# Performance work log

Measured on AMD Instinct MI355X. Metric: run time of the kernel, lower is better.

## Reference

```python
import jax, jax.numpy as jnp
import numpy as np

B, NPB, K = 8, 4096, 16            # batches, points per batch, knn neighbors
IN_FEAT, OUT_FEAT, N_HEADS = 64, 64, 8
N = B * NPB
HD = OUT_FEAT // N_HEADS           # per-head dim (linear_w output width)
EPS = 1e-5


def _bn(x, g, b):
    # LayerNorm1d == BatchNorm1d over channel dim with stats across (N, k)
    m = jnp.mean(x, axis=(0, 1), keepdims=True)
    v = jnp.mean((x - m) ** 2, axis=(0, 1), keepdims=True)
    return (x - m) * jax.lax.rsqrt(v + EPS) * g + b


def _knn_idx(feat):
    # per-batch self-KNN in feature space (torch_geometric.nn.knn(x, x, k, batch, batch))
    f = feat.reshape(B, NPB, -1)
    sq = jnp.sum(f * f, axis=-1)                               # [B, n]
    d = sq[:, :, None] + sq[:, None, :] - 2.0 * jnp.einsum('bnc,bmc->bnm', f, f)
    _, idx = jax.lax.top_k(-d, K)                              # [B, n, K]
    idx = idx + (jnp.arange(B) * NPB)[:, None, None]           # global indices
    return idx.reshape(N, K)


def setup_inputs() -> dict:
    key = jax.random.key(0)
    ks = jax.random.split(key, 12)
    s = 0.05
    return {
        "p": jax.random.normal(ks[0], (N, 3), dtype=jnp.float32),
        "x": jax.random.normal(ks[1], (N, IN_FEAT), dtype=jnp.float32),
        "o": jnp.full((B,), NPB, dtype=jnp.int32),
        # q/k/v projections
        "wq": jax.random.normal(ks[2], (IN_FEAT, OUT_FEAT)) * s, "bq": jnp.zeros((OUT_FEAT,)),
        "wk": jax.random.normal(ks[3], (IN_FEAT, OUT_FEAT)) * s, "bk": jnp.zeros((OUT_FEAT,)),
        "wv": jax.random.normal(ks[4], (IN_FEAT, OUT_FEAT)) * s, "bv": jnp.zeros((OUT_FEAT,)),
        # linear_p: Linear(3,3) -> BN(3) -> ReLU -> Linear(3, out)
        "wp1": jax.random.normal(ks[5], (3, 3)) * s, "bp1": jnp.zeros((3,)),
        "gp": jnp.ones((3,)), "btp": jnp.zeros((3,)),
        "wp2": jax.random.normal(ks[6], (3, OUT_FEAT)) * s, "bp2": jnp.zeros((OUT_FEAT,)),
        # linear_w: BN(mid) -> ReLU -> Linear(mid, hd) -> BN(hd) -> ReLU -> Linear(hd, hd)
        "g1": jnp.ones((OUT_FEAT,)), "bt1": jnp.zeros((OUT_FEAT,)),
        "ww1": jax.random.normal(ks[7], (OUT_FEAT, HD)) * s, "bw1": jnp.zeros((HD,)),
        "g2": jnp.ones((HD,)), "bt2": jnp.zeros((HD,)),
        "ww2": jax.random.normal(ks[8], (HD, HD)) * s, "bw2": jnp.zeros((HD,)),
    }


def reference(p, x, o, wq, bq, wk, bk, wv, bv, wp1, bp1, gp, btp, wp2, bp2,
              g1, bt1, ww1, bw1, g2, bt2, ww2, bw2):
    # o encodes equal-size batches (NPB each); structure is baked into the knn helper.
    xq = x @ wq + bq                      # [N, mid]
    xk = x @ wk + bk                      # [N, mid]
    xv = x @ wv + bv                      # [N, out]
    idx_k = _knn_idx(xk)                  # KNN in k-feature space
    idx_v = _knn_idx(xv)                  # separate KNN in v-feature space (as in source)
    xk_g = xk[idx_k]                      # [N, K, mid]
    p_rel = p[idx_k] - p[:, None, :]      # grouped relative xyz [N, K, 3]
    xv_g = xv[idx_v]                      # [N, K, out]
    # position encoding MLP
    h = p_rel @ wp1 + bp1
    h = jax.nn.relu(_bn(h, gp, btp))
    p_r = h @ wp2 + bp2                   # [N, K, out]; einops.reduce with i=1 is identity
    # relation features and attention-weight MLP
    r = xk_g - xq[:, None, :] + p_r       # [N, K, mid]
    w = jax.nn.relu(_bn(r, g1, bt1)) @ ww1 + bw1
    w = jax.nn.relu(_bn(w, g2, bt2)) @ ww2 + bw2   # [N, K, HD]
    w = jax.nn.softmax(w, axis=1)         # softmax over neighbors
    comb = (xv_g + p_r).reshape(N, K, N_HEADS, HD)
    out = jnp.einsum('ntsi,nti->nsi', comb, w).reshape(N, OUT_FEAT)
    return out
```

## Files before the change

kernel.cpp:

```cpp
#include <hip/hip_runtime.h>
#include <hip/hip_bf16.h>

typedef __hip_bfloat16 bf16;

#define NPTS  32768
#define NPB   4096
#define NPAIR (NPTS*16)
#define IMASK 32767
#define EPSB  1e-5f

#define O_WQ  0
#define O_BQ  4096
#define O_WK  4160
#define O_BK  8256
#define O_WV  8320
#define O_BV  12416
#define O_WP1 12480
#define O_BP1 12489
#define O_GP  12492
#define O_BTP 12495
#define O_WP2 12498
#define O_BP2 12690
#define O_G1  12754
#define O_BT1 12818
#define O_WW1 12882
#define O_BW1 13394
#define O_G2  13402
#define O_BT2 13410
#define O_WW2 13418
#define O_BW2 13482
#define NPRM  13490

__device__ __forceinline__ float b2f(bf16 v){ return __bfloat162float(v); }
__device__ __forceinline__ float u16f(unsigned short u){ return __uint_as_float(((unsigned)u)<<16); }
__device__ __forceinline__ float ldany(const void* p, long long i, int f32){
    return f32 ? ((const float*)p)[i] : b2f(((const bf16*)p)[i]);
}

__device__ __forceinline__ void split2(float x, unsigned &h, unsigned &m){
    unsigned u  = __float_as_uint(x);
    unsigned hr = (u + 0x7FFFu + ((u>>16)&1u)) & 0xFFFF0000u;
    float xm = x - __uint_as_float(hr);
    h = hr >> 16;
    m = __float_as_uint(xm) >> 16;
}

__device__ __forceinline__ void gll16(const void* g, void* l){
    __builtin_amdgcn_global_load_lds((const __attribute__((address_space(1))) unsigned*)(g),
                                     (__attribute__((address_space(3))) unsigned*)(l), 16, 0, 0);
}
__device__ __forceinline__ void gll4(const void* g, void* l){
    __builtin_amdgcn_global_load_lds((const __attribute__((address_space(1))) unsigned*)(g),
                                     (__attribute__((address_space(3))) unsigned*)(l), 4, 0, 0);
}

struct P20 { const void* p[20]; };

__global__ __launch_bounds__(256) void k_conv(P20 t, const void* __restrict__ p,
                                              const void* __restrict__ x, const void* __restrict__ wq0,
                                              float* __restrict__ prm, float* __restrict__ p32,
                                              int* __restrict__ flags)
{
    __shared__ float red[2][4];
    const unsigned short* xu = (const unsigned short*)x;
    const unsigned short* wu = (const unsigned short*)wq0;
    const int tid = threadIdx.x, lane = tid & 63, wvi = tid >> 6;
    float mx = fabsf(u16f(xu[tid]));
    float mw = fabsf(u16f(wu[tid]));
    for (int off = 32; off; off >>= 1){
        mx = fmaxf(mx, __shfl_down(mx, off));
        mw = fmaxf(mw, __shfl_down(mw, off));
    }
    if (lane == 0){ red[0][wvi] = mx; red[1][wvi] = mw; }
    __syncthreads();
    const float ax = fmaxf(fmaxf(red[0][0], red[0][1]), fmaxf(red[0][2], red[0][3]));
    const float aw = fmaxf(fmaxf(red[1][0], red[1][1]), fmaxf(red[1][2], red[1][3]));
    const int f0 = (ax > 1e6f) ? 1 : 0;
    const int f1 = (aw > 1e6f) ? 1 : 0;
    if (blockIdx.x == 0 && tid == 0){ flags[0] = f0; flags[1] = f1; }
    const int i = blockIdx.x*256 + tid;
    if (i < NPRM){
        const int sz[20] = {4096,64,4096,64,4096,64,9,3,3,3,192,64,64,64,512,8,8,8,64,8};
        int seg = 0, rem = i;
        while (rem >= sz[seg]){ rem -= sz[seg]; ++seg; }
        prm[i] = ldany(t.p[seg], rem, f1);
    } else {
        const int j = i - NPRM;
        if (j < NPTS*3) p32[j] = ldany(p, j, f0);
    }
}

__global__ __launch_bounds__(192) void k_proj(
    const void* __restrict__ x, const int* __restrict__ flags,
    const float* __restrict__ prm,
    float* __restrict__ xq, float* __restrict__ xk, float* __restrict__ xv,
    float* __restrict__ sqk, float* __restrict__ sqv,
    unsigned* __restrict__ hkp, unsigned* __restrict__ mkp,
    unsigned* __restrict__ hvp, unsigned* __restrict__ mvp)
{
    const int tid = threadIdx.x, lane = tid & 63, wvi = tid >> 6;
    const int f32 = flags[0];
    const int OW = (wvi==0) ? O_WQ : (wvi==1) ? O_WK : O_WV;
    const int OB = (wvi==0) ? O_BQ : (wvi==1) ? O_BK : O_BV;
    float Wc[64];
    #pragma unroll
    for (int k = 0; k < 64; ++k) Wc[k] = prm[OW + k*64 + lane];
    const float bias = prm[OB + lane];
    float* outp = (wvi==0) ? xq : (wvi==1) ? xk : xv;
    const int ptbase = blockIdx.x*32;
    for (int it = 0; it < 32; ++it){
        const int pt = ptbase + it;
        float xl = ldany(x, (long long)pt*64 + lane, f32);
        float acc = bias;
        #pragma unroll
        for (int k = 0; k < 64; ++k) acc += __shfl(xl, k)*Wc[k];
        outp[(size_t)pt*64 + lane] = acc;
        if (wvi){
            unsigned h16, m16; split2(acc, h16, m16);
            unsigned hn = __shfl_down(h16,1), mn = __shfl_down(m16,1);
            if (!(lane & 1)){
                const int u = lane >> 3, pos = u ^ (pt & 7);
                const size_t gi = (size_t)pt*32 + pos*4 + ((lane & 7) >> 1);
                if (wvi == 1){ hkp[gi] = h16 | (hn<<16);  mkp[gi] = m16 | (mn<<16); }
                else         { hvp[gi] = h16 | (hn<<16);  mvp[gi] = m16 | (mn<<16); }
            }
            float s = acc*acc;
            for (int off=32; off; off>>=1) s += __shfl_down(s, off);
            if (lane == 0){ if (wvi == 1) sqk[pt] = s; else sqv[pt] = s; }
        }
    }
}


using bfrag  = __attribute__((ext_vector_type(8))) short;
using f32x16 = __attribute__((ext_vector_type(16))) float;

__device__ __forceinline__ int lds_sw(int row, int unit){
    return (row<<6) + (((unit ^ row) & 7)<<3);
}

__global__ __launch_bounds__(256, 4) void k_knn_part(
    const float* __restrict__ featk, const float* __restrict__ featv,
    const unsigned* __restrict__ hkp, const unsigned* __restrict__ mkp,
    const unsigned* __restrict__ hvp, const unsigned* __restrict__ mvp,
    const float* __restrict__ sqk, const float* __restrict__ sqv,
    const float* __restrict__ p32, const float* __restrict__ prm,
    int* __restrict__ idx_k, int* __restrict__ idx_v,
    float* __restrict__ part1)
{
    __shared__ __attribute__((aligned(16))) unsigned char smem[34048];
    __shared__ float bn1red[4][6];
    unsigned short* Ch = (unsigned short*)smem;
    unsigned short* Cm = (unsigned short*)(smem + 8192);
    float* Dt  = (float*)(smem + 16384);
    float* sqC = (float*)(smem + 16384 + 17408);
    unsigned long long* Lbuf = (unsigned long long*)smem;

    const int tid = threadIdx.x;
    const int swz = ((int)blockIdx.x & 7) * 128 + ((int)blockIdx.x >> 3);
    const int kid = swz >> 9;
    const int bid = swz & 511;
    const float*    feat = kid ? featv : featk;
    const float*    sq   = kid ? sqv  : sqk;
    const unsigned* hpl  = kid ? hvp : hkp;
    const unsigned* mpl  = kid ? mvp : mkp;
    const int b  = bid >> 6;
    const int qt = bid & 63;
    const int q0 = b*NPB + qt*64;
    const int cb = b*NPB;

    const int lane = tid & 63, wv = tid >> 6;
    const int qg = wv >> 1, cg = wv & 1;
    const int l31 = lane & 31, hi = lane >> 5;
    const int selq = (wv << 4) + (lane >> 2);
    const int sub  = lane & 3;
    const int owner = lane & ~3;

    bfrag qh[4], qm[4];
    {
        const int qr = q0 + (qg<<5) + l31;
        #pragma unroll
        for (int ks = 0; ks < 4; ++ks){
            const int u = ks*2 + hi;
            const int pos = u ^ (qr & 7);
            union { uint4 u4; bfrag v; } ch, cm;
            ch.u4 = *(const uint4*)&hpl[(size_t)qr*32 + pos*4];
            cm.u4 = *(const uint4*)&mpl[(size_t)qr*32 + pos*4];
            qh[ks] = ch.v; qm[ks] = cm.v;
        }
    }

    float d5[5]; int i5[5];
    #pragma unroll
    for (int i=0;i<5;++i){ d5[i] = 3.4e38f; i5[i] = 0; }

    const unsigned* hrowA = hpl + (size_t)cb*32 + (size_t)tid*4;
    const unsigned* mrowA = mpl + (size_t)cb*32 + (size_t)tid*4;

    #define STAGE(CHN) { \
        const size_t co = (size_t)(CHN)*2048; \
        gll16(hrowA + co,        (void*)&Ch[8*tid]); \
        gll16(hrowA + co + 1024, (void*)&Ch[8*tid + 2048]); \
        gll16(mrowA + co,        (void*)&Cm[8*tid]); \
        gll16(mrowA + co + 1024, (void*)&Cm[8*tid + 2048]); \
        if (tid < 64) gll4(sq + cb + (CHN)*64 + tid, (void*)&sqC[tid]); \
    }

    #define MFMA_PHASE() { \
        const int cd = (cg<<5) + l31; \
        f32x16 acc = {0.f,0.f,0.f,0.f,0.f,0.f,0.f,0.f,0.f,0.f,0.f,0.f,0.f,0.f,0.f,0.f}; \
        _Pragma("unroll") \
        for (int ks = 0; ks < 4; ++ks){ \
            const int u = ks*2 + hi; \
            union { uint4 u4; bfrag v; } bh, bm; \
            bh.u4 = *(const uint4*)&Ch[lds_sw(cd, u)]; \
            bm.u4 = *(const uint4*)&Cm[lds_sw(cd, u)]; \
            acc = __builtin_amdgcn_mfma_f32_32x32x16_bf16(qm[ks], bm.v, acc, 0, 0, 0); \
            acc = __builtin_amdgcn_mfma_f32_32x32x16_bf16(qh[ks], bm.v, acc, 0, 0, 0); \
            acc = __builtin_amdgcn_mfma_f32_32x32x16_bf16(qm[ks], bh.v, acc, 0, 0, 0); \
            acc = __builtin_amdgcn_mfma_f32_32x32x16_bf16(qh[ks], bh.v, acc, 0, 0, 0); \
        } \
        const float sc = sqC[(cg<<5) + l31]; \
        _Pragma("unroll") \
        for (int i = 0; i < 16; ++i){ \
            const int row = (qg<<5) + (i&3) + 8*(i>>2) + 4*hi; \
            Dt[row*68 + (cg<<5) + l31] = sc - 2.f*acc[i]; \
        } }

    STAGE(0)
    __syncthreads();

    for (int chn = 0; chn < 64; ++chn){
        MFMA_PHASE()
        __syncthreads();
        if (chn + 1 < 64) STAGE(chn+1)
        {
            float worst = __shfl(d5[4], owner+3);
            unsigned m16 = 0;
            const int rowoff = selq*68 + sub*16;
            #pragma unroll
            for (int r = 0; r < 4; ++r){
                float4 v = *(const float4*)&Dt[rowoff + 4*r];
                m16 |= (v.x < worst ? 1u : 0u) << (4*r+0);
                m16 |= (v.y < worst ? 1u : 0u) << (4*r+1);
                m16 |= (v.z < worst ? 1u : 0u) << (4*r+2);
                m16 |= (v.w < worst ? 1u : 0u) << (4*r+3);
            }
            unsigned ma = __shfl(m16, owner+0), mb = __shfl(m16, owner+1);
            unsigned mc = __shfl(m16, owner+2), md = __shfl(m16, owner+3);
            unsigned long long m = (unsigned long long)ma
                                 | ((unsigned long long)mb << 16)
                                 | ((unsigned long long)mc << 32)
                                 | ((unsigned long long)md << 48);
            const int qrow = selq*68;
            const int c0 = cb + chn*64;
            const int prevlane = (lane - 1) & 63;
            while (m){
                int c = (int)__builtin_ctzll(m); m &= m - 1;
                float d = Dt[qrow + c];
                int gi = c0 + c;
                float pl = __shfl(d5[4], prevlane);
                int   pi = __shfl(i5[4], prevlane);
                bool takePrev = (sub != 0) && (pl > d);
                float v  = takePrev ? pl : d;
                int   vi = takePrev ? pi : gi;
                #pragma unroll
                for (int i = 4; i >= 1; --i){
                    bool sh   = d5[i-1] > v;
                    bool here = !sh && (d5[i] > v);
                    d5[i] = sh ? d5[i-1] : (here ? v  : d5[i]);
                    i5[i] = sh ? i5[i-1] : (here ? vi : i5[i]);
                }
                bool h0 = d5[0] > v;
                d5[0] = h0 ? v  : d5[0];
                i5[0] = h0 ? vi : i5[0];
            }
        }
        __syncthreads();
    }
    #undef MFMA_PHASE
    #undef STAGE

    unsigned long long k5[5];
    {
        const float* qrow = feat + (size_t)(q0 + selq)*64;
        #pragma unroll
        for (int s = 0; s < 5; ++s){
            const int gi = i5[s];
            const float* crow = feat + (size_t)gi*64;
            float acc = 0.f;
            #pragma unroll
            for (int k4 = 0; k4 < 16; ++k4){
                float4 qv = *(const float4*)&qrow[4*k4];
                float4 cv = *(const float4*)&crow[4*k4];
                acc += qv.x*cv.x; acc += qv.y*cv.y; acc += qv.z*cv.z; acc += qv.w*cv.w;
            }
            float d = sq[gi] - 2.f*acc;
            unsigned ud = __float_as_uint(d);
            ud ^= (ud & 0x80000000u) ? 0xFFFFFFFFu : 0x80000000u;
            k5[s] = ((unsigned long long)ud << 32) | (unsigned)gi;
        }
    }
    #pragma unroll
    for (int pass = 0; pass < 5; ++pass){
        #pragma unroll
        for (int i = (pass & 1); i + 1 < 5; i += 2){
            unsigned long long a = k5[i], bb = k5[i+1];
            bool sw = a > bb;
            k5[i]   = sw ? bb : a;
            k5[i+1] = sw ? a : bb;
        }
    }
    __syncthreads();
    #pragma unroll
    for (int j = 0; j < 5; ++j) Lbuf[(size_t)tid*6 + j] = k5[j];
    Lbuf[(size_t)tid*6 + 5] = ~0ull;
    __syncthreads();
    int fi[16];
    #pragma unroll
    for (int i = 0; i < 16; ++i) fi[i] = 0;
    if (sub == 0){
        const unsigned long long* L0 = &Lbuf[(size_t)(tid+0)*6];
        const unsigned long long* L1 = &Lbuf[(size_t)(tid+1)*6];
        const unsigned long long* L2 = &Lbuf[(size_t)(tid+2)*6];
        const unsigned long long* L3 = &Lbuf[(size_t)(tid+3)*6];
        int p0 = 0, p1 = 0, p2 = 0, p3 = 0;
        #pragma unroll
        for (int o = 0; o < 16; ++o){
            unsigned long long b0 = L0[p0], b1v = L1[p1], b2v = L2[p2], b3v = L3[p3];
            unsigned long long m01 = (b0  < b1v) ? b0  : b1v;  int s01 = (b0  < b1v) ? 0 : 1;
            unsigned long long m23 = (b2v < b3v) ? b2v : b3v;  int s23 = (b2v < b3v) ? 2 : 3;
            unsigned long long mm  = (m01 < m23) ? m01 : m23;  int ss  = (m01 < m23) ? s01 : s23;
            fi[o] = (int)(unsigned)(mm & 0xFFFFFFFFull);
            if      (ss == 0) ++p0;
            else if (ss == 1) ++p1;
            else if (ss == 2) ++p2;
            else              ++p3;
        }
        int* idx_out = kid ? idx_v : idx_k;
        #pragma unroll
        for (int i4 = 0; i4 < 4; ++i4)
            *(int4*)&idx_out[(size_t)(q0+selq)*16 + 4*i4] =
                make_int4(fi[4*i4], fi[4*i4+1], fi[4*i4+2], fi[4*i4+3]);
    }

    if (kid == 0){
        const float w00=prm[O_WP1+0], w01=prm[O_WP1+1], w02=prm[O_WP1+2];
        const float w10=prm[O_WP1+3], w11=prm[O_WP1+4], w12=prm[O_WP1+5];
        const float w20=prm[O_WP1+6], w21=prm[O_WP1+7], w22=prm[O_WP1+8];
        const float bb0=prm[O_BP1+0], bb1=prm[O_BP1+1], bb2=prm[O_BP1+2];
        const size_t gq = (size_t)(q0 + selq);
        const float px=p32[gq*3+0], py=p32[gq*3+1], pz=p32[gq*3+2];
        float s0=0.f,s1=0.f,s2=0.f,t0=0.f,t1=0.f,t2=0.f;
        #pragma unroll
        for (int o = 0; o < 16; ++o){
            int gi = __shfl(fi[o], owner);
            if ((o & 3) == sub){
                const int j = gi & IMASK;
                float rx = p32[j*3+0]-px, ry = p32[j*3+1]-py, rz = p32[j*3+2]-pz;
                float h0 = bb0 + rx*w00 + ry*w10 + rz*w20;
                float h1 = bb1 + rx*w01 + ry*w11 + rz*w21;
                float h2 = bb2 + rx*w02 + ry*w12 + rz*w22;
                s0+=h0; s1+=h1; s2+=h2; t0+=h0*h0; t1+=h1*h1; t2+=h2*h2;
            }
        }
        #pragma unroll
        for (int off = 1; off < 64; off <<= 1){
            s0+=__shfl_down(s0,off); s1+=__shfl_down(s1,off); s2+=__shfl_down(s2,off);
            t0+=__shfl_down(t0,off); t1+=__shfl_down(t1,off); t2+=__shfl_down(t2,off);
        }
        if (lane == 0){
            bn1red[wv][0]=s0; bn1red[wv][1]=s1; bn1red[wv][2]=s2;
            bn1red[wv][3]=t0; bn1red[wv][4]=t1; bn1red[wv][5]=t2;
        }
        __syncthreads();
        if (tid < 6)
            part1[(size_t)tid*512 + bid] =
                bn1red[0][tid]+bn1red[1][tid]+bn1red[2][tid]+bn1red[3][tid];
    }
}

__global__ __launch_bounds__(256) void k_bnred_par(
    const float* __restrict__ part, int G, int C,
    const float* __restrict__ gamma, const float* __restrict__ beta,
    float* __restrict__ aff, float invCount)
{
    __shared__ float rs[4], rq[4];
    const int c = blockIdx.x;
    const int tid = threadIdx.x;
    float s = 0.f, q = 0.f;
    for (int g = tid; g < G; g += 256){
        s += part[(size_t)c*G + g];
        q += part[(size_t)(C+c)*G + g];
    }
    for (int off=32; off; off>>=1){ s += __shfl_down(s,off); q += __shfl_down(q,off); }
    if ((tid & 63) == 0){ rs[tid>>6] = s; rq[tid>>6] = q; }
    __syncthreads();
    if (tid == 0){
        float S = rs[0]+rs[1]+rs[2]+rs[3], Q = rq[0]+rq[1]+rq[2]+rq[3];
        float mean = S*invCount;
        float var  = fmaxf(Q*invCount - mean*mean, 0.f);
        float sc = gamma[c] * rsqrtf(var + EPSB);
        aff[c]   = sc;
        aff[C+c] = beta[c] - mean*sc;
    }
}

__global__ __launch_bounds__(256) void k_rstats(
    const float* __restrict__ p32,
    const float* __restrict__ xq, const float* __restrict__ xk, const int* __restrict__ idx_k,
    const float* __restrict__ bn1aff, const float* __restrict__ prm,
    float* __restrict__ part2)
{
    const int tid = threadIdx.x, lane = tid & 63, wvi = tid >> 6;
    const float wa = prm[O_WP2+lane], wb = prm[O_WP2+64+lane], wc = prm[O_WP2+128+lane];
    const float bpc = prm[O_BP2+lane];
    const float w00=prm[O_WP1+0], w01=prm[O_WP1+1], w02=prm[O_WP1+2];
    const float w10=prm[O_WP1+3], w11=prm[O_WP1+4], w12=prm[O_WP1+5];
    const float w20=prm[O_WP1+6], w21=prm[O_WP1+7], w22=prm[O_WP1+8];
    const float bb0=prm[O_BP1+0], bb1=prm[O_BP1+1], bb2=prm[O_BP1+2];
    const float sc0=bn1aff[0], sc1=bn1aff[1], sc2=bn1aff[2];
    const float sh0=bn1aff[3], sh1=bn1aff[4], sh2=bn1aff[5];
    const int base = (blockIdx.x*4 + wvi) * 64;
    float asum=0.f, asq=0.f;
    float px=0.f, py=0.f, pz=0.f, xql=0.f;
    for (int e4 = 0; e4 < 16; ++e4){
        const int gb = base + e4*4;
        if ((gb & 15) == 0){
            const int n = gb >> 4;
            px=p32[n*3+0]; py=p32[n*3+1]; pz=p32[n*3+2];
            xql = xq[(size_t)n*64+lane];
        }
        int4 jj = *(const int4*)&idx_k[gb];
        int j[4] = { jj.x & IMASK, jj.y & IMASK, jj.z & IMASK, jj.w & IMASK };
        float kx[4], qx[4][3];
        #pragma unroll
        for (int u=0;u<4;++u){
            qx[u][0]=p32[j[u]*3+0]; qx[u][1]=p32[j[u]*3+1]; qx[u][2]=p32[j[u]*3+2];
            kx[u] = xk[(size_t)j[u]*64+lane];
        }
        #pragma unroll
        for (int u=0;u<4;++u){
            float rx = qx[u][0]-px, ry = qx[u][1]-py, rz = qx[u][2]-pz;
            float h0 = bb0 + rx*w00 + ry*w10 + rz*w20;
            float h1 = bb1 + rx*w01 + ry*w11 + rz*w21;
            float h2 = bb2 + rx*w02 + ry*w12 + rz*w22;
            float r0 = fmaxf(h0*sc0+sh0, 0.f), r1 = fmaxf(h1*sc1+sh1,0.f), r2 = fmaxf(h2*sc2+sh2,0.f);
            float pr = r0*wa + r1*wb + r2*wc + bpc;
            float rv = kx[u] - xql + pr;
            asum += rv; asq += rv*rv;
        }
    }
    __shared__ float red[4][128];
    red[wvi][lane] = asum; red[wvi][64+lane] = asq;
    __syncthreads();
    if (tid < 128)
        part2[(size_t)tid*2048 + blockIdx.x] = red[0][tid]+red[1][tid]+red[2][tid]+red[3][tid];
}

__global__ __launch_bounds__(256) void k_wstats(
    const float* __restrict__ p32,
    const float* __restrict__ xq, const float* __restrict__ xk, const int* __restrict__ idx_k,
    const float* __restrict__ bn1aff, const float* __restrict__ prm,
    const float* __restrict__ bn2aff, float* __restrict__ wbuf, float* __restrict__ part3)
{
    __shared__ float4 PRW[64];
    __shared__ float2 SS2[64];
    __shared__ float4 W1A[64], W1B[64];
    const int tid = threadIdx.x;
    if (tid < 64){
        PRW[tid] = make_float4(prm[O_WP2+tid], prm[O_WP2+64+tid], prm[O_WP2+128+tid], prm[O_BP2+tid]);
        SS2[tid] = make_float2(bn2aff[tid], bn2aff[64+tid]);
        W1A[tid] = make_float4(prm[O_WW1+tid*8+0],prm[O_WW1+tid*8+1],prm[O_WW1+tid*8+2],prm[O_WW1+tid*8+3]);
        W1B[tid] = make_float4(prm[O_WW1+tid*8+4],prm[O_WW1+tid*8+5],prm[O_WW1+tid*8+6],prm[O_WW1+tid*8+7]);
    }
    __syncthreads();
    const int g = blockIdx.x*256 + tid;
    const int n = g >> 4;
    const int j = idx_k[g] & IMASK;
    const float w00=prm[O_WP1+0], w01=prm[O_WP1+1], w02=prm[O_WP1+2];
    const float w10=prm[O_WP1+3], w11=prm[O_WP1+4], w12=prm[O_WP1+5];
    const float w20=prm[O_WP1+6], w21=prm[O_WP1+7], w22=prm[O_WP1+8];
    const float bb0=prm[O_BP1+0], bb1=prm[O_BP1+1], bb2=prm[O_BP1+2];
    const float sc0=bn1aff[0], sc1=bn1aff[1], sc2=bn1aff[2];
    const float sh0=bn1aff[3], sh1=bn1aff[4], sh2=bn1aff[5];
    float rx = p32[j*3+0] - p32[n*3+0];
    float ry = p32[j*3+1] - p32[n*3+1];
    float rz = p32[j*3+2] - p32[n*3+2];
    float h0 = bb0 + rx*w00 + ry*w10 + rz*w20;
    float h1 = bb1 + rx*w01 + ry*w11 + rz*w21;
    float h2 = bb2 + rx*w02 + ry*w12 + rz*w22;
    float r0 = fmaxf(h0*sc0+sh0, 0.f), r1 = fmaxf(h1*sc1+sh1,0.f), r2 = fmaxf(h2*sc2+sh2,0.f);
    float wacc[8];
    #pragma unroll
    for (int i=0;i<8;++i) wacc[i] = prm[O_BW1+i];
    const float4* kr = (const float4*)(xk + (size_t)j*64);
    const float4* qr = (const float4*)(xq + (size_t)n*64);
    #pragma unroll
    for (int c4=0;c4<16;++c4){
        float4 kv = kr[c4], qv = qr[c4];
        float kvv[4] = {kv.x,kv.y,kv.z,kv.w};
        float qvv[4] = {qv.x,qv.y,qv.z,qv.w};
        #pragma unroll
        for (int d=0; d<4; ++d){
            int c = 4*c4 + d;
            float4 pw = PRW[c]; float2 ss = SS2[c];
            float pr = r0*pw.x + r1*pw.y + r2*pw.z + pw.w;
            float rr = kvv[d] - qvv[d] + pr;
            float y = fmaxf(rr*ss.x + ss.y, 0.f);
            float4 wA = W1A[c], wB = W1B[c];
            wacc[0]+=y*wA.x; wacc[1]+=y*wA.y; wacc[2]+=y*wA.z; wacc[3]+=y*wA.w;
            wacc[4]+=y*wB.x; wacc[5]+=y*wB.y; wacc[6]+=y*wB.z; wacc[7]+=y*wB.w;
        }
    }
    *(float4*)&wbuf[(size_t)g*8]   = make_float4(wacc[0],wacc[1],wacc[2],wacc[3]);
    *(float4*)&wbuf[(size_t)g*8+4] = make_float4(wacc[4],wacc[5],wacc[6],wacc[7]);
    float st[16];
    #pragma unroll
    for (int i=0;i<8;++i){ st[i]=wacc[i]; st[8+i]=wacc[i]*wacc[i]; }
    for (int off=32; off; off>>=1){
        #pragma unroll
        for (int k=0;k<16;++k) st[k] += __shfl_down(st[k], off);
    }
    __shared__ float red[4][16];
    const int lane = tid&63, wvi = tid>>6;
    if (lane==0){
        #pragma unroll
        for (int k=0;k<16;++k) red[wvi][k]=st[k];
    }
    __syncthreads();
    if (tid < 16)
        part3[(size_t)tid*2048 + blockIdx.x] = red[0][tid]+red[1][tid]+red[2][tid]+red[3][tid];
}

__global__ __launch_bounds__(256) void k_out(
    const float* __restrict__ p32, const float* __restrict__ xv,
    const int* __restrict__ idx_k, const int* __restrict__ idx_v,
    const float* __restrict__ bn1aff, const float* __restrict__ prm,
    const float* __restrict__ wbuf, const float* __restrict__ bn3aff,
    const int* __restrict__ flags, void* __restrict__ out)
{
    const int tid = threadIdx.x, lane = tid & 63, wvi = tid >> 6;
    const int n = blockIdx.x*4 + wvi;
    const int f32 = flags[0];
    const float w00=prm[O_WP1+0], w01=prm[O_WP1+1], w02=prm[O_WP1+2];
    const float w10=prm[O_WP1+3], w11=prm[O_WP1+4], w12=prm[O_WP1+5];
    const float w20=prm[O_WP1+6], w21=prm[O_WP1+7], w22=prm[O_WP1+8];
    const float bb0=prm[O_BP1+0], bb1=prm[O_BP1+1], bb2=prm[O_BP1+2];
    const float sc0=bn1aff[0], sc1=bn1aff[1], sc2=bn1aff[2];
    const float sh0=bn1aff[3], sh1=bn1aff[4], sh2=bn1aff[5];
    const float wa=prm[O_WP2+lane], wb=prm[O_WP2+64+lane], wc=prm[O_WP2+128+lane];
    const float bpc=prm[O_BP2+lane];
    const int i = lane & 7;
    float s3[8], t3[8], w2col[8];
    #pragma unroll
    for (int m=0;m<8;++m){
        s3[m]=bn3aff[m]; t3[m]=bn3aff[8+m];
        w2col[m]=prm[O_WW2+m*8+i];
    }
    const float bw2i = prm[O_BW2+i];
    const float px=p32[n*3+0], py=p32[n*3+1], pz=p32[n*3+2];
    float comb[16], wf[16];
    #pragma unroll
    for (int t=0;t<16;++t){
        const int g = n*16 + t;
        const int jk = idx_k[g] & IMASK;
        const int jv = idx_v[g] & IMASK;
        float rx=p32[jk*3+0]-px, ry=p32[jk*3+1]-py, rz=p32[jk*3+2]-pz;
        float h0=bb0+rx*w00+ry*w10+rz*w20;
        float h1=bb1+rx*w01+ry*w11+rz*w21;
        float h2=bb2+rx*w02+ry*w12+rz*w22;
        float r0=fmaxf(h0*sc0+sh0,0.f), r1=fmaxf(h1*sc1+sh1,0.f), r2=fmaxf(h2*sc2+sh2,0.f);
        float pr=r0*wa+r1*wb+r2*wc+bpc;
        float4 wA = *(const float4*)&wbuf[(size_t)g*8];
        float4 wB = *(const float4*)&wbuf[(size_t)g*8+4];
        float wm[8] = {wA.x,wA.y,wA.z,wA.w,wB.x,wB.y,wB.z,wB.w};
        float acc = bw2i;
        #pragma unroll
        for (int m=0;m<8;++m){
            float y3 = fmaxf(wm[m]*s3[m]+t3[m],0.f);
            acc += y3*w2col[m];
        }
        wf[t]=acc;
        comb[t]=xv[(size_t)jv*64+lane]+pr;
    }
    float mx = wf[0];
    #pragma unroll
    for (int t=1;t<16;++t) mx = fmaxf(mx, wf[t]);
    float ssum=0.f, osum=0.f;
    #pragma unroll
    for (int t=0;t<16;++t){ float e = __expf(wf[t]-mx); ssum += e; osum += e*comb[t]; }
    const float v = osum / ssum;
    if (f32) ((float*)out)[(size_t)n*64+lane] = v;
    else     ((bf16*)out)[(size_t)n*64+lane] = __float2bfloat16(v);
}

extern "C" void kernel_launch(void* const* d_in, const int* in_sizes, int n_in,
                              void* d_out, int out_size, void* d_ws, size_t ws_size,
                              hipStream_t stream)
{
    const void* p  = d_in[0];
    const void* x  = d_in[1];
    P20 prms;
    for (int i = 0; i < 20; ++i) prms.p[i] = d_in[3+i];

    float* W = (float*)d_ws;
    float* xqf    = W + 0;
    float* xkf    = W + 2097152;
    float* xvf    = W + 4194304;
    float* sqk    = W + 6291456;
    float* sqv    = W + 6324224;
    int*   idx_k  = (int*)(W + 6356992);
    int*   idx_v  = (int*)(W + 6881280);
    float* p32    = W + 7405568;
    float* prm    = W + 7503872;
    float* part1  = W + 7517376;
    float* part2  = W + 7529664;
    float* part3  = W + 7791808;
    float* bn1aff = W + 7824576;
    float* bn2aff = W + 7824592;
    float* bn3aff = W + 7824720;
    int*   flags  = (int*)(W + 7824736);
    unsigned* hkp = (unsigned*)(W + 7824752);
    unsigned* mkp = (unsigned*)(W + 7824752 + 1048576);
    unsigned* hvp = (unsigned*)(W + 7824752 + 2097152);
    unsigned* mvp = (unsigned*)(W + 7824752 + 3145728);
    float* wbuf   = W + 7824752;

    const float invP = 1.f / (float)NPAIR;

    k_conv<<<(NPRM + NPTS*3 + 255)/256,256,0,stream>>>(prms, p, x, d_in[3], prm, p32, flags);
    k_proj<<<1024,192,0,stream>>>(x, flags, prm, xqf,xkf,xvf, sqk,sqv, hkp,mkp,hvp,mvp);
    k_knn_part<<<1024,256,0,stream>>>(xkf, xvf, hkp,mkp,hvp,mvp, sqk, sqv,
                                      p32, prm, idx_k, idx_v, part1);
    k_bnred_par<<<3,256,0,stream>>>(part1, 512, 3, prm+O_GP, prm+O_BTP, bn1aff, invP);
    k_rstats<<<2048,256,0,stream>>>(p32, xqf, xkf, idx_k, bn1aff, prm, part2);
    k_bnred_par<<<64,256,0,stream>>>(part2, 2048, 64, prm+O_G1, prm+O_BT1, bn2aff, invP);
    k_wstats<<<2048,256,0,stream>>>(p32, xqf, xkf, idx_k, bn1aff, prm, bn2aff, wbuf, part3);
    k_bnred_par<<<8,256,0,stream>>>(part3, 2048, 8, prm+O_G2, prm+O_BT2, bn3aff, invP);
    k_out<<<8192,256,0,stream>>>(p32, xvf, idx_k, idx_v, bn1aff, prm,
                                 wbuf, bn3aff, flags, d_out);
}
```

Baseline: 591.9 us.

## Remove BN reduction kernels by using atomic stats and per-block affine derivation

Drops the three small k_bnred_par launches. BN2/BN3 partial sums are now accumulated with atomicAdd into small zeroed buffers instead of per-block partial arrays. Each consumer kernel derives the BN affine parameters itself, and the BN1 stats are re-reduced from the 512 partials in every block. This removes kernel launches and serialization gaps, at the cost of redundant per-block reductions, atomic contention on 128/16 addresses, and nondeterministic float summation order.

```diff
diff --git a/kernel.cpp b/kernel.cpp
--- a/kernel.cpp
+++ b/kernel.cpp
@@ -54,12 +54,36 @@
                                      (__attribute__((address_space(3))) unsigned*)(l), 4, 0, 0);
 }
 
+#define DERIVE_BN1(part1, prm, invP, aff, tid)                                    \
+    {                                                                             \
+        if ((tid) < 64){                                                          \
+            const int lane_ = (tid);                                              \
+            _Pragma("unroll")                                                     \
+            for (int s2 = 0; s2 < 6; ++s2){                                       \
+                float v = 0.f;                                                    \
+                for (int g = lane_; g < 512; g += 64) v += (part1)[s2*512 + g];   \
+                for (int off=32; off; off>>=1) v += __shfl_down(v, off);          \
+                if (lane_ == 0) (aff)[s2] = v;                                    \
+            }                                                                     \
+        }                                                                         \
+        __syncthreads();                                                          \
+        if ((tid) < 3){                                                           \
+            float mean_ = (aff)[(tid)]*(invP);                                    \
+            float var_  = fmaxf((aff)[3+(tid)]*(invP) - mean_*mean_, 0.f);        \
+            float sc_ = (prm)[O_GP+(tid)] * rsqrtf(var_ + EPSB);                  \
+            float sh_ = (prm)[O_BTP+(tid)] - mean_*sc_;                           \
+            (aff)[(tid)] = sc_; (aff)[3+(tid)] = sh_;                             \
+        }                                                                         \
+        __syncthreads();                                                          \
+    }
+
 struct P20 { const void* p[20]; };
 
 __global__ __launch_bounds__(256) void k_conv(P20 t, const void* __restrict__ p,
                                               const void* __restrict__ x, const void* __restrict__ wq0,
                                               float* __restrict__ prm, float* __restrict__ p32,
-                                              int* __restrict__ flags)
+                                              int* __restrict__ flags,
+                                              float* __restrict__ bn2part, float* __restrict__ bn3part)
 {
     __shared__ float red[2][4];
     const unsigned short* xu = (const unsigned short*)x;
@@ -77,7 +101,11 @@
     const float aw = fmaxf(fmaxf(red[1][0], red[1][1]), fmaxf(red[1][2], red[1][3]));
     const int f0 = (ax > 1e6f) ? 1 : 0;
     const int f1 = (aw > 1e6f) ? 1 : 0;
-    if (blockIdx.x == 0 && tid == 0){ flags[0] = f0; flags[1] = f1; }
+    if (blockIdx.x == 0){
+        if (tid == 0){ flags[0] = f0; flags[1] = f1; }
+        if (tid < 128) bn2part[tid] = 0.f;
+        if (tid < 16)  bn3part[tid] = 0.f;
+    }
     const int i = blockIdx.x*256 + tid;
     if (i < NPRM){
         const int sz[20] = {4096,64,4096,64,4096,64,9,3,3,3,192,64,64,64,512,8,8,8,64,8};
@@ -130,7 +158,6 @@
         }
     }
 }
-
 
 using bfrag  = __attribute__((ext_vector_type(8))) short;
 using f32x16 = __attribute__((ext_vector_type(16))) float;
@@ -380,47 +407,24 @@
     }
 }
 
-__global__ __launch_bounds__(256) void k_bnred_par(
-    const float* __restrict__ part, int G, int C,
-    const float* __restrict__ gamma, const float* __restrict__ beta,
-    float* __restrict__ aff, float invCount)
-{
-    __shared__ float rs[4], rq[4];
-    const int c = blockIdx.x;
-    const int tid = threadIdx.x;
-    float s = 0.f, q = 0.f;
-    for (int g = tid; g < G; g += 256){
-        s += part[(size_t)c*G + g];
-        q += part[(size_t)(C+c)*G + g];
-    }
-    for (int off=32; off; off>>=1){ s += __shfl_down(s,off); q += __shfl_down(q,off); }
-    if ((tid & 63) == 0){ rs[tid>>6] = s; rq[tid>>6] = q; }
-    __syncthreads();
-    if (tid == 0){
-        float S = rs[0]+rs[1]+rs[2]+rs[3], Q = rq[0]+rq[1]+rq[2]+rq[3];
-        float mean = S*invCount;
-        float var  = fmaxf(Q*invCount - mean*mean, 0.f);
-        float sc = gamma[c] * rsqrtf(var + EPSB);
-        aff[c]   = sc;
-        aff[C+c] = beta[c] - mean*sc;
-    }
-}
-
 __global__ __launch_bounds__(256) void k_rstats(
     const float* __restrict__ p32,
     const float* __restrict__ xq, const float* __restrict__ xk, const int* __restrict__ idx_k,
-    const float* __restrict__ bn1aff, const float* __restrict__ prm,
-    float* __restrict__ part2)
+    const float* __restrict__ part1, const float* __restrict__ prm,
+    float* __restrict__ bn2part, float invP)
 {
+    __shared__ float aff1[6];
+    __shared__ float red[4][128];
     const int tid = threadIdx.x, lane = tid & 63, wvi = tid >> 6;
+    DERIVE_BN1(part1, prm, invP, aff1, tid)
+    const float sc0=aff1[0], sc1=aff1[1], sc2=aff1[2];
+    const float sh0=aff1[3], sh1=aff1[4], sh2=aff1[5];
     const float wa = prm[O_WP2+lane], wb = prm[O_WP2+64+lane], wc = prm[O_WP2+128+lane];
     const float bpc = prm[O_BP2+lane];
     const float w00=prm[O_WP1+0], w01=prm[O_WP1+1], w02=prm[O_WP1+2];
     const float w10=prm[O_WP1+3], w11=prm[O_WP1+4], w12=prm[O_WP1+5];
     const float w20=prm[O_WP1+6], w21=prm[O_WP1+7], w22=prm[O_WP1+8];
     const float bb0=prm[O_BP1+0], bb1=prm[O_BP1+1], bb2=prm[O_BP1+2];
-    const float sc0=bn1aff[0], sc1=bn1aff[1], sc2=bn1aff[2];
-    const float sh0=bn1aff[3], sh1=bn1aff[4], sh2=bn1aff[5];
     const int base = (blockIdx.x*4 + wvi) * 64;
     float asum=0.f, asq=0.f;
     float px=0.f, py=0.f, pz=0.f, xql=0.f;
@@ -451,30 +455,38 @@
             asum += rv; asq += rv*rv;
         }
     }
-    __shared__ float red[4][128];
     red[wvi][lane] = asum; red[wvi][64+lane] = asq;
     __syncthreads();
     if (tid < 128)
-        part2[(size_t)tid*2048 + blockIdx.x] = red[0][tid]+red[1][tid]+red[2][tid]+red[3][tid];
+        atomicAdd(&bn2part[tid], red[0][tid]+red[1][tid]+red[2][tid]+red[3][tid]);
 }
 
 __global__ __launch_bounds__(256) void k_wstats(
     const float* __restrict__ p32,
     const float* __restrict__ xq, const float* __restrict__ xk, const int* __restrict__ idx_k,
-    const float* __restrict__ bn1aff, const float* __restrict__ prm,
-    const float* __restrict__ bn2aff, float* __restrict__ wbuf, float* __restrict__ part3)
+    const float* __restrict__ part1, const float* __restrict__ prm,
+    const float* __restrict__ bn2part, float* __restrict__ wbuf,
+    float* __restrict__ bn3part, float invP)
 {
+    __shared__ float aff1[6];
     __shared__ float4 PRW[64];
     __shared__ float2 SS2[64];
     __shared__ float4 W1A[64], W1B[64];
+    __shared__ float red[4][16];
     const int tid = threadIdx.x;
+    DERIVE_BN1(part1, prm, invP, aff1, tid)
     if (tid < 64){
         PRW[tid] = make_float4(prm[O_WP2+tid], prm[O_WP2+64+tid], prm[O_WP2+128+tid], prm[O_BP2+tid]);
-        SS2[tid] = make_float2(bn2aff[tid], bn2aff[64+tid]);
+        float mean = bn2part[tid]*invP;
+        float var  = fmaxf(bn2part[64+tid]*invP - mean*mean, 0.f);
+        float sc = prm[O_G1+tid] * rsqrtf(var + EPSB);
+        SS2[tid] = make_float2(sc, prm[O_BT1+tid] - mean*sc);
         W1A[tid] = make_float4(prm[O_WW1+tid*8+0],prm[O_WW1+tid*8+1],prm[O_WW1+tid*8+2],prm[O_WW1+tid*8+3]);
         W1B[tid] = make_float4(prm[O_WW1+tid*8+4],prm[O_WW1+tid*8+5],prm[O_WW1+tid*8+6],prm[O_WW1+tid*8+7]);
     }
     __syncthreads();
+    const float sc0=aff1[0], sc1=aff1[1], sc2=aff1[2];
+    const float sh0=aff1[3], sh1=aff1[4], sh2=aff1[5];
     const int g = blockIdx.x*256 + tid;
     const int n = g >> 4;
     const int j = idx_k[g] & IMASK;
@@ -482,8 +494,6 @@
     const float w10=prm[O_WP1+3], w11=prm[O_WP1+4], w12=prm[O_WP1+5];
     const float w20=prm[O_WP1+6], w21=prm[O_WP1+7], w22=prm[O_WP1+8];
     const float bb0=prm[O_BP1+0], bb1=prm[O_BP1+1], bb2=prm[O_BP1+2];
-    const float sc0=bn1aff[0], sc1=bn1aff[1], sc2=bn1aff[2];
-    const float sh0=bn1aff[3], sh1=bn1aff[4], sh2=bn1aff[5];
     float rx = p32[j*3+0] - p32[n*3+0];
     float ry = p32[j*3+1] - p32[n*3+1];
     float rz = p32[j*3+2] - p32[n*3+2];
@@ -522,7 +532,6 @@
         #pragma unroll
         for (int k=0;k<16;++k) st[k] += __shfl_down(st[k], off);
     }
-    __shared__ float red[4][16];
     const int lane = tid&63, wvi = tid>>6;
     if (lane==0){
         #pragma unroll
@@ -530,32 +539,43 @@
     }
     __syncthreads();
     if (tid < 16)
-        part3[(size_t)tid*2048 + blockIdx.x] = red[0][tid]+red[1][tid]+red[2][tid]+red[3][tid];
+        atomicAdd(&bn3part[tid], red[0][tid]+red[1][tid]+red[2][tid]+red[3][tid]);
 }
 
 __global__ __launch_bounds__(256) void k_out(
     const float* __restrict__ p32, const float* __restrict__ xv,
     const int* __restrict__ idx_k, const int* __restrict__ idx_v,
-    const float* __restrict__ bn1aff, const float* __restrict__ prm,
-    const float* __restrict__ wbuf, const float* __restrict__ bn3aff,
-    const int* __restrict__ flags, void* __restrict__ out)
+    const float* __restrict__ part1, const float* __restrict__ prm,
+    const float* __restrict__ wbuf, const float* __restrict__ bn3part,
+    const int* __restrict__ flags, void* __restrict__ out, float invP)
 {
+    __shared__ float aff1[6];
+    __shared__ float aff3[16];
     const int tid = threadIdx.x, lane = tid & 63, wvi = tid >> 6;
+    DERIVE_BN1(part1, prm, invP, aff1, tid)
+    if (tid < 8){
+        float mean = bn3part[tid]*invP;
+        float var  = fmaxf(bn3part[8+tid]*invP - mean*mean, 0.f);
+        float sc = prm[O_G2+tid] * rsqrtf(var + EPSB);
+        aff3[tid]   = sc;
+        aff3[8+tid] = prm[O_BT2+tid] - mean*sc;
+    }
+    __syncthreads();
+    const float sc0=aff1[0], sc1=aff1[1], sc2=aff1[2];
+    const float sh0=aff1[3], sh1=aff1[4], sh2=aff1[5];
     const int n = blockIdx.x*4 + wvi;
     const int f32 = flags[0];
     const float w00=prm[O_WP1+0], w01=prm[O_WP1+1], w02=prm[O_WP1+2];
     const float w10=prm[O_WP1+3], w11=prm[O_WP1+4], w12=prm[O_WP1+5];
     const float w20=prm[O_WP1+6], w21=prm[O_WP1+7], w22=prm[O_WP1+8];
     const float bb0=prm[O_BP1+0], bb1=prm[O_BP1+1], bb2=prm[O_BP1+2];
-    const float sc0=bn1aff[0], sc1=bn1aff[1], sc2=bn1aff[2];
-    const float sh0=bn1aff[3], sh1=bn1aff[4], sh2=bn1aff[5];
     const float wa=prm[O_WP2+lane], wb=prm[O_WP2+64+lane], wc=prm[O_WP2+128+lane];
     const float bpc=prm[O_BP2+lane];
     const int i = lane & 7;
     float s3[8], t3[8], w2col[8];
     #pragma unroll
     for (int m=0;m<8;++m){
-        s3[m]=bn3aff[m]; t3[m]=bn3aff[8+m];
+        s3[m]=aff3[m]; t3[m]=aff3[8+m];
         w2col[m]=prm[O_WW2+m*8+i];
     }
     const float bw2i = prm[O_BW2+i];
@@ -615,12 +635,9 @@
     float* p32    = W + 7405568;
     float* prm    = W + 7503872;
     float* part1  = W + 7517376;
-    float* part2  = W + 7529664;
-    float* part3  = W + 7791808;
-    float* bn1aff = W + 7824576;
-    float* bn2aff = W + 7824592;
-    float* bn3aff = W + 7824720;
-    int*   flags  = (int*)(W + 7824736);
+    float* bn2part= W + 7529664;
+    float* bn3part= W + 7529824;
+    int*   flags  = (int*)(W + 7529856);
     unsigned* hkp = (unsigned*)(W + 7824752);
     unsigned* mkp = (unsigned*)(W + 7824752 + 1048576);
     unsigned* hvp = (unsigned*)(W + 7824752 + 2097152);
@@ -629,15 +646,14 @@
 
     const float invP = 1.f / (float)NPAIR;
 
-    k_conv<<<(NPRM + NPTS*3 + 255)/256,256,0,stream>>>(prms, p, x, d_in[3], prm, p32, flags);
+    k_conv<<<(NPRM + NPTS*3 + 255)/256,256,0,stream>>>(prms, p, x, d_in[3], prm, p32,
+                                                       flags, bn2part, bn3part);
     k_proj<<<1024,192,0,stream>>>(x, flags, prm, xqf,xkf,xvf, sqk,sqv, hkp,mkp,hvp,mvp);
     k_knn_part<<<1024,256,0,stream>>>(xkf, xvf, hkp,mkp,hvp,mvp, sqk, sqv,
                                       p32, prm, idx_k, idx_v, part1);
-    k_bnred_par<<<3,256,0,stream>>>(part1, 512, 3, prm+O_GP, prm+O_BTP, bn1aff, invP);
-    k_rstats<<<2048,256,0,stream>>>(p32, xqf, xkf, idx_k, bn1aff, prm, part2);
-    k_bnred_par<<<64,256,0,stream>>>(part2, 2048, 64, prm+O_G1, prm+O_BT1, bn2aff, invP);
-    k_wstats<<<2048,256,0,stream>>>(p32, xqf, xkf, idx_k, bn1aff, prm, bn2aff, wbuf, part3);
-    k_bnred_par<<<8,256,0,stream>>>(part3, 2048, 8, prm+O_G2, prm+O_BT2, bn3aff, invP);
-    k_out<<<8192,256,0,stream>>>(p32, xvf, idx_k, idx_v, bn1aff, prm,
-                                 wbuf, bn3aff, flags, d_out);
-}
+    k_rstats<<<2048,256,0,stream>>>(p32, xqf, xkf, idx_k, part1, prm, bn2part, invP);
+    k_wstats<<<2048,256,0,stream>>>(p32, xqf, xkf, idx_k, part1, prm, bn2part,
+                                    wbuf, bn3part, invP);
+    k_out<<<8192,256,0,stream>>>(p32, xvf, idx_k, idx_v, part1, prm,
+                                 wbuf, bn3part, flags, d_out, invP);
+}
```

After: 707.3 us. 19.5% more time.
